# Performance work log

Measured on AMD Instinct MI355X. Metric: run time of the kernel, lower is better.

## Reference

```python
import jax, jax.numpy as jnp
import numpy as np

DEPTH = 3  # chemprop default message passing depth


def setup_inputs() -> dict:
    key = jax.random.key(0)
    ks = jax.random.split(key, 10)
    n_atoms, n_bonds, max_nb, n_mols = 50000, 100000, 6, 2000
    atom_fdim, bond_fdim, hidden = 133, 147, 300
    f_atoms = jax.random.normal(ks[0], (n_atoms, atom_fdim), dtype=jnp.float32)
    f_bonds = jax.random.normal(ks[1], (n_bonds, bond_fdim), dtype=jnp.float32)
    a2b = jax.random.randint(ks[2], (n_atoms, max_nb), 0, n_bonds, dtype=jnp.int32)
    b2a = jax.random.randint(ks[3], (n_bonds,), 0, n_atoms, dtype=jnp.int32)
    b2revb = jax.random.randint(ks[4], (n_bonds,), 0, n_bonds, dtype=jnp.int32)
    mol_id = jnp.sort(jax.random.randint(ks[5], (n_atoms,), 0, n_mols, dtype=jnp.int32))
    W_i = jax.random.normal(ks[6], (bond_fdim, hidden), dtype=jnp.float32) * 0.05
    W_h = jax.random.normal(ks[7], (hidden, hidden), dtype=jnp.float32) * 0.05
    W_o = jax.random.normal(ks[8], (atom_fdim + hidden, hidden), dtype=jnp.float32) * 0.05
    b_o = jnp.zeros((hidden,), dtype=jnp.float32)
    return {"f_atoms": f_atoms, "f_bonds": f_bonds, "a2b": a2b, "b2a": b2a,
            "b2revb": b2revb, "mol_id": mol_id, "n_mols": n_mols,
            "W_i": W_i, "W_h": W_h, "W_o": W_o, "b_o": b_o}


def reference(f_atoms, f_bonds, a2b, b2a, b2revb, mol_id, n_mols, W_i, W_h, W_o, b_o):
    act = jax.nn.relu
    # W_i: bond features -> hidden; message init
    inp = f_bonds @ W_i                      # [n_bonds, h]
    message = act(inp)
    for _ in range(DEPTH - 1):
        nei = message[a2b]                    # [n_atoms, max_nb, h] gather
        a_message = nei.sum(axis=1)           # [n_atoms, h]
        rev = message[b2revb]                 # [n_bonds, h]
        message = a_message[b2a] - rev        # [n_bonds, h]
        message = act(inp + message @ W_h)
    # final atom readout
    a_message = message[a2b].sum(axis=1)      # [n_atoms, h]
    a_input = jnp.concatenate([f_atoms, a_message], axis=1)  # [n_atoms, fa+h]
    atom_hiddens = act(a_input @ W_o + b_o)   # [n_atoms, h]
    # ragged per-molecule mean (a_scope loop -> segment mean)
    sums = jax.ops.segment_sum(atom_hiddens, mol_id, num_segments=n_mols)
    counts = jax.ops.segment_sum(jnp.ones((atom_hiddens.shape[0],), dtype=atom_hiddens.dtype), mol_id, num_segments=n_mols)
    mol_vecs = jnp.where(counts[:, None] > 0, sums / jnp.maximum(counts, 1.0)[:, None], 0.0)
    return mol_vecs
```

## Files before the change

### kernel.cpp

```cpp
#include <hip/hip_runtime.h>
#include <cstddef>

#define H 300
#define RS 304
#define MAXNB 6
#define ASTR 312

typedef __attribute__((ext_vector_type(8)))  short bf16x8;
typedef __attribute__((ext_vector_type(16))) float f32x16;

__device__ __forceinline__ float bf2f(unsigned short u) {
    return __uint_as_float(((unsigned int)u) << 16);
}
__device__ __forceinline__ unsigned short f2bf(float f) {
    unsigned int u = __float_as_uint(f);
    u += 0x7FFFu + ((u >> 16) & 1u);
    return (unsigned short)(u >> 16);
}
__device__ __forceinline__ unsigned int sub2bf(unsigned int a, unsigned int b) {
    float d0 = bf2f((unsigned short)(a & 0xFFFFu)) - bf2f((unsigned short)(b & 0xFFFFu));
    float d1 = bf2f((unsigned short)(a >> 16))     - bf2f((unsigned short)(b >> 16));
    return (unsigned int)f2bf(d0) | ((unsigned int)f2bf(d1) << 16);
}
__device__ __forceinline__ unsigned int relu2(unsigned int w) {
    unsigned int r = w;
    if (w & 0x80000000u) r &= 0x0000FFFFu;
    if (w & 0x00008000u) r &= 0xFFFF0000u;
    return r;
}
__device__ __forceinline__ uint4 relu4(uint4 v) {
    v.x = relu2(v.x); v.y = relu2(v.y); v.z = relu2(v.z); v.w = relu2(v.w);
    return v;
}
__device__ __forceinline__ uint4 subpack4(uint4 a, uint4 b) {
    uint4 r;
    r.x = sub2bf(a.x, b.x); r.y = sub2bf(a.y, b.y);
    r.z = sub2bf(a.z, b.z); r.w = sub2bf(a.w, b.w);
    return r;
}


template<int S>
__global__ void __launch_bounds__(256)
pack_a_f32_c(const float* __restrict__ src, unsigned short* __restrict__ dst,
             int M, int K)
{
    __shared__ unsigned short sm[64 * 152];
    const int m0 = blockIdx.x * 64;
    const int r = threadIdx.x >> 2;
    const int q = threadIdx.x & 3;
    int mv = m0 + r; if (mv >= M) mv = M - 1;
    const float* rowF = src + (size_t)mv * K;
#pragma unroll
    for (int i = 0; i < (S * 4 + 3) / 4; ++i) {
        int c = q + i * 4;
        if (c * 4 < S * 16) {
            unsigned short h[4];
#pragma unroll
            for (int e = 0; e < 4; ++e) {
                int k = c * 4 + e;
                h[e] = (k < K) ? f2bf(rowF[k]) : (unsigned short)0;
            }
            uint2 o;
            o.x = (unsigned int)h[0] | ((unsigned int)h[1] << 16);
            o.y = (unsigned int)h[2] | ((unsigned int)h[3] << 16);
            *(uint2*)&sm[r * 152 + c * 4] = o;
        }
    }
    __syncthreads();
    for (int j = threadIdx.x; j < 2 * S * 64; j += 256) {
        int lane = j & 63;
        int t = j >> 6;
        int s = t % S;
        int mb2 = t / S;
        uint4 v = *(const uint4*)&sm[(mb2 * 32 + (lane & 31)) * 152 + s * 16 + (lane >> 5) * 8];
        int m_blk = blockIdx.x * 2 + mb2;
        *(uint4*)&dst[((size_t)(m_blk * S + s) * 64 + lane) * 8] = v;
    }
}

__device__ __forceinline__ void
pack_b_body(int g, const float* __restrict__ src1, const float* __restrict__ src2,
            unsigned short* __restrict__ dst, int K1, int S1, int K2, int SB)
{
    if (g >= 10 * SB * 64) return;
    int lane = g & 63;
    int t = g >> 6;
    int s = t % SB;
    int n_blk = t / SB;
    int n = n_blk * 32 + (lane & 31);
    unsigned int w[4];
#pragma unroll
    for (int p = 0; p < 4; ++p) {
        unsigned short h[2];
#pragma unroll
        for (int e = 0; e < 2; ++e) {
            int kf = s * 16 + (lane >> 5) * 8 + p * 2 + e;
            float v = 0.0f;
            if (n < H) {
                if (s < S1) {
                    if (kf < K1) v = src1[(size_t)kf * H + n];
                } else {
                    int k2 = kf - S1 * 16;
                    if (k2 < K2) v = src2[(size_t)k2 * H + n];
                }
            }
            h[e] = f2bf(v);
        }
        w[p] = (unsigned int)h[0] | ((unsigned int)h[1] << 16);
    }
    *(uint4*)&dst[(size_t)g * 8] = make_uint4(w[0], w[1], w[2], w[3]);
}

__global__ void __launch_bounds__(256)
pack_b_all(const float* __restrict__ Wi, const float* __restrict__ Wh,
           const float* __restrict__ Wo,
           unsigned short* __restrict__ wih, unsigned short* __restrict__ wh19,
           unsigned short* __restrict__ wo, int bond_fdim, int atom_fdim)
{
    const int B0 = (10 * 30 * 64 + 255) / 256;
    const int B1 = (10 * 19 * 64 + 255) / 256;
    int b = blockIdx.x;
    if (b < B0) {
        pack_b_body(b * 256 + threadIdx.x, Wi, Wh, wih, bond_fdim, 10, H, 30);
    } else if (b < B0 + B1) {
        pack_b_body((b - B0) * 256 + threadIdx.x, Wh, Wh, wh19, H, 19, 0, 19);
    } else {
        pack_b_body((b - B0 - B1) * 256 + threadIdx.x, Wo,
                    Wo + (size_t)atom_fdim * H, wo, atom_fdim, 9, H, 29);
    }
}

template<int RELU>
__global__ void __launch_bounds__(256)
aggregate_row(const unsigned short* __restrict__ msg, const int* __restrict__ a2b,
              unsigned short* __restrict__ amsg, int n_atoms)
{
    int gid = blockIdx.x * 256 + threadIdx.x;
    int total = n_atoms * 38;
    if (gid >= total) return;
    int atom = gid / 38;
    int g8 = gid - atom * 38;
    const int* nb = a2b + atom * MAXNB;
    float sum[8] = {};
#pragma unroll
    for (int j = 0; j < MAXNB; ++j) {
        int b = nb[j];
        uint4 v = *(const uint4*)&msg[(size_t)b * RS + g8 * 8];
        if (RELU) v = relu4(v);
        unsigned int ww[4] = {v.x, v.y, v.z, v.w};
#pragma unroll
        for (int p = 0; p < 4; ++p) {
            sum[p * 2]     += bf2f((unsigned short)(ww[p] & 0xFFFFu));
            sum[p * 2 + 1] += bf2f((unsigned short)(ww[p] >> 16));
        }
    }
    unsigned int ow[4];
#pragma unroll
    for (int p = 0; p < 4; ++p)
        ow[p] = (unsigned int)f2bf(sum[p * 2]) | ((unsigned int)f2bf(sum[p * 2 + 1]) << 16);
    *(uint4*)&amsg[(size_t)atom * RS + g8 * 8] = make_uint4(ow[0], ow[1], ow[2], ow[3]);
}

template<int S1, int S2, int SBL, int MODE, int RELUMSG>
__global__ void __launch_bounds__(640, 8)
gemm_fused(const unsigned short* __restrict__ A1,
           const unsigned short* __restrict__ amsg,
           const unsigned short* __restrict__ msg,
           const int* __restrict__ b2a, const int* __restrict__ b2revb,
           const unsigned short* __restrict__ Bp,
           const float* __restrict__ bias,
           const unsigned short* __restrict__ inp_add,
           const float* __restrict__ Adense, int Kd,
           unsigned short* __restrict__ out, int M)
{
    __shared__ __align__(16) unsigned short smem[64 * ASTR];

    const int lane  = threadIdx.x & 63;
    const int w     = threadIdx.x >> 6;
    const int mrow  = lane & 31;
    const int quad  = lane >> 5;
    const int m0    = blockIdx.x * 64;

    if (threadIdx.x < 512) {
        const int r = threadIdx.x >> 3;
        const int q = threadIdx.x & 7;
        int mm = m0 + r;
        int mv = (mm < M) ? mm : 0;
        if (MODE == 0) {
            if (mm >= M) mv = M - 1;
            const float* rowF = Adense + (size_t)mv * Kd;
#pragma unroll
            for (int i = 0; i < 5; ++i) {
                int c = q + i * 8;
                if (c * 4 < S2 * 16) {
                    unsigned short h[4];
#pragma unroll
                    for (int e = 0; e < 4; ++e) {
                        int k = c * 4 + e;
                        h[e] = (k < Kd) ? f2bf(rowF[k]) : (unsigned short)0;
                    }
                    uint2 o;
                    o.x = (unsigned int)h[0] | ((unsigned int)h[1] << 16);
                    o.y = (unsigned int)h[2] | ((unsigned int)h[3] << 16);
                    *(uint2*)&smem[r * ASTR + c * 4] = o;
                }
            }
        } else if (MODE == 3) {
            const int* nb = b2a + mv * MAXNB;
#pragma unroll
            for (int i = 0; i < 5; ++i) {
                int c = q + i * 8;
                if (c < 38) {
                    float sum[8] = {};
#pragma unroll
                    for (int j = 0; j < MAXNB; ++j) {
                        uint4 v = *(const uint4*)&msg[(size_t)nb[j] * RS + c * 8];
                        unsigned int ww[4] = {v.x, v.y, v.z, v.w};
#pragma unroll
                        for (int p = 0; p < 4; ++p) {
                            sum[p * 2]     += bf2f((unsigned short)(ww[p] & 0xFFFFu));
                            sum[p * 2 + 1] += bf2f((unsigned short)(ww[p] >> 16));
                        }
                    }
                    unsigned int ow[4];
#pragma unroll
                    for (int p = 0; p < 4; ++p)
                        ow[p] = (unsigned int)f2bf(sum[p * 2]) |
                                ((unsigned int)f2bf(sum[p * 2 + 1]) << 16);
                    *(uint4*)&smem[r * ASTR + c * 8] = make_uint4(ow[0], ow[1], ow[2], ow[3]);
                }
            }
        } else {
            const unsigned short* rowA;
            const unsigned short* rowM = nullptr;
            if (MODE == 1) {
                rowA = amsg + (size_t)b2a[mv] * RS;
                rowM = msg  + (size_t)b2revb[mv] * RS;
            } else {
                rowA = amsg + (size_t)mv * RS;
            }
#pragma unroll
            for (int i = 0; i < 5; ++i) {
                int c = q + i * 8;
                if (c < 38) {
                    uint4 o;
                    if (MODE == 1) {
                        uint4 va = *(const uint4*)(rowA + c * 8);
                        uint4 vm = *(const uint4*)(rowM + c * 8);
                        if (RELUMSG) vm = relu4(vm);
                        o = subpack4(va, vm);
                    } else {
                        o = *(const uint4*)(rowA + c * 8);
                    }
                    *(uint4*)&smem[r * ASTR + c * 8] = o;
                }
            }
        }
    }
    __syncthreads();

    f32x16 acc_lo, acc_hi;
#pragma unroll
    for (int i = 0; i < 16; ++i) { acc_lo[i] = 0.0f; acc_hi[i] = 0.0f; }

    const unsigned short* pa1_lo = (S1 > 0)
        ? (A1 + ((size_t)(blockIdx.x * 2 + 0) * S1 * 64 + lane) * 8) : nullptr;
    const unsigned short* pa1_hi = (S1 > 0)
        ? (A1 + ((size_t)(blockIdx.x * 2 + 1) * S1 * 64 + lane) * 8) : nullptr;
    const unsigned short* pb = Bp + ((size_t)w * SBL * 64 + lane) * 8;

    constexpr int STOT = S1 + S2;

    auto loadA = [&](int s, const unsigned short* pa1x, int half) -> bf16x8 {
        if (S1 > 0 && s < S1) return *(const bf16x8*)(pa1x + (size_t)s * 512);
        return *(const bf16x8*)&smem[((half << 5) + mrow) * ASTR + (s - S1) * 16 + quad * 8];
    };

    bf16x8 b0, b1;
    b0 = *(const bf16x8*)(pb);
    if (STOT > 1) b1 = *(const bf16x8*)(pb + 512);

#pragma unroll
    for (int s = 0; s < STOT; s += 2) {
        bf16x8 a_lo = loadA(s, pa1_lo, 0);
        bf16x8 a_hi = loadA(s, pa1_hi, 1);
        acc_lo = __builtin_amdgcn_mfma_f32_32x32x16_bf16(a_lo, b0, acc_lo, 0, 0, 0);
        acc_hi = __builtin_amdgcn_mfma_f32_32x32x16_bf16(a_hi, b0, acc_hi, 0, 0, 0);
        if (s + 2 < STOT) b0 = *(const bf16x8*)(pb + (size_t)(s + 2) * 512);
        if (s + 1 < STOT) {
            bf16x8 a_lo2 = loadA(s + 1, pa1_lo, 0);
            bf16x8 a_hi2 = loadA(s + 1, pa1_hi, 1);
            acc_lo = __builtin_amdgcn_mfma_f32_32x32x16_bf16(a_lo2, b1, acc_lo, 0, 0, 0);
            acc_hi = __builtin_amdgcn_mfma_f32_32x32x16_bf16(a_hi2, b1, acc_hi, 0, 0, 0);
            if (s + 3 < STOT) b1 = *(const bf16x8*)(pb + (size_t)(s + 3) * 512);
        }
    }

    __syncthreads();

    {
        int col = w * 32 + mrow;
        if (col < 308) {
#pragma unroll
            for (int r = 0; r < 16; ++r) {
                int row = (r & 3) + 8 * (r >> 2) + 4 * quad;
                smem[row * 308 + col] = f2bf(acc_lo[r]);
            }
#pragma unroll
            for (int r = 0; r < 16; ++r) {
                int row = 32 + (r & 3) + 8 * (r >> 2) + 4 * quad;
                smem[row * 308 + col] = f2bf(acc_hi[r]);
            }
        }
    }
    __syncthreads();

    for (int idx = threadIdx.x; idx < 64 * 76; idx += 640) {
        int row = idx / 76, gcol = idx - row * 76;
        int mm = m0 + row;
        if (mm >= M) continue;
        int c0 = gcol * 4;
        uint2 raw = *(const uint2*)&smem[row * 308 + c0];
        uint2 o;
        if (MODE == 0) {
            o = raw;
        } else {
            unsigned short h[4] = {(unsigned short)(raw.x & 0xFFFFu), (unsigned short)(raw.x >> 16),
                                   (unsigned short)(raw.y & 0xFFFFu), (unsigned short)(raw.y >> 16)};
            float v[4];
#pragma unroll
            for (int e = 0; e < 4; ++e) v[e] = bf2f(h[e]);
            if (MODE == 1) {
                uint2 iv = *(const uint2*)&inp_add[(size_t)mm * RS + c0];
                v[0] += bf2f((unsigned short)(iv.x & 0xFFFFu));
                v[1] += bf2f((unsigned short)(iv.x >> 16));
                v[2] += bf2f((unsigned short)(iv.y & 0xFFFFu));
                v[3] += bf2f((unsigned short)(iv.y >> 16));
            } else {
#pragma unroll
                for (int e = 0; e < 4; ++e) v[e] += (c0 + e < H) ? bias[c0 + e] : 0.0f;
            }
#pragma unroll
            for (int e = 0; e < 4; ++e) h[e] = f2bf(fmaxf(v[e], 0.0f));
            o.x = (unsigned int)h[0] | ((unsigned int)h[1] << 16);
            o.y = (unsigned int)h[2] | ((unsigned int)h[3] << 16);
        }
        *(uint2*)&out[(size_t)mm * RS + c0] = o;
    }
}

__global__ void __launch_bounds__(128)
segmean_kernel(const unsigned short* __restrict__ ah,
               const int* __restrict__ mol_id, int n_atoms,
               float* __restrict__ out)
{
    int m = blockIdx.x;
    int lo = 0, hi = n_atoms;
    while (lo < hi) { int mid = (lo + hi) >> 1; if (mol_id[mid] < m) lo = mid + 1; else hi = mid; }
    int start = lo;
    hi = n_atoms;
    while (lo < hi) { int mid = (lo + hi) >> 1; if (mol_id[mid] < m + 1) lo = mid + 1; else hi = mid; }
    int end = lo;

    int c = threadIdx.x;
    float a0 = 0.f, a1 = 0.f, a2 = 0.f;
    for (int a = start; a < end; ++a) {
        const unsigned short* row = ah + (size_t)a * RS;
        a0 += bf2f(row[c]);
        a1 += bf2f(row[c + 128]);
        if (c < H - 256) a2 += bf2f(row[c + 256]);
    }
    float inv = (end > start) ? 1.0f / (float)(end - start) : 0.0f;
    float* orow = out + (size_t)m * H;
    orow[c] = a0 * inv;
    orow[c + 128] = a1 * inv;
    if (c < H - 256) orow[c + 256] = a2 * inv;
}

extern "C" void kernel_launch(void* const* d_in, const int* in_sizes, int n_in,
                              void* d_out, int out_size, void* d_ws, size_t ws_size,
                              hipStream_t stream)
{
    const float* f_atoms = (const float*)d_in[0];
    const float* f_bonds = (const float*)d_in[1];
    const int*   a2b     = (const int*)d_in[2];
    const int*   b2a     = (const int*)d_in[3];
    const int*   b2revb  = (const int*)d_in[4];
    const int*   mol_id  = (const int*)d_in[5];
    const float* W_i     = (const float*)d_in[7];
    const float* W_h     = (const float*)d_in[8];
    const float* W_o     = (const float*)d_in[9];
    const float* b_o     = (const float*)d_in[10];

    const int n_atoms   = in_sizes[5];
    const int n_bonds   = in_sizes[3];
    const int atom_fdim = in_sizes[0] / n_atoms;
    const int bond_fdim = in_sizes[1] / n_bonds;
    const int n_mols    = out_size / H;

    const int gAtoms  = (n_atoms + 63) / 64;
    const int gBonds  = (n_bonds + 63) / 64;

    const size_t bondsRS = (size_t)n_bonds * RS;
    const size_t atomsRS = (size_t)n_atoms * RS;
    const size_t wihSz   = 10 * 30 * 512;
    const size_t woSz    = 10 * 29 * 512;
    const size_t wh19Sz  = 10 * 19 * 512;

    unsigned short* inp  = (unsigned short*)d_ws;
    unsigned short* msgB = inp  + bondsRS;
    unsigned short* amsg = msgB + bondsRS;
    unsigned short* wih  = amsg + atomsRS;
    unsigned short* wo   = wih  + wihSz;
    unsigned short* wh19 = wo   + woSz;
    unsigned short* ah   = wh19 + wh19Sz;
    unsigned short* fap  = msgB;

    dim3 blk(256);
    dim3 gblk(640);
    const int aggBlocks = (n_atoms * 38 + 255) / 256;
    const int packBlocks = (10 * 30 * 64 + 255) / 256 + (10 * 19 * 64 + 255) / 256
                         + (10 * 29 * 64 + 255) / 256;

    pack_b_all<<<packBlocks, blk, 0, stream>>>(W_i, W_h, W_o, wih, wh19, wo,
                                               bond_fdim, atom_fdim);

    gemm_fused<0, 10, 30, 0, 0><<<gBonds, gblk, 0, stream>>>(
        nullptr, nullptr, nullptr, nullptr, nullptr, wih, nullptr, nullptr,
        f_bonds, bond_fdim, inp, n_bonds);

    aggregate_row<1><<<aggBlocks, blk, 0, stream>>>(inp, a2b, amsg, n_atoms);
    gemm_fused<0, 19, 19, 1, 1><<<gBonds, gblk, 0, stream>>>(
        nullptr, amsg, inp, b2a, b2revb, wh19, nullptr, inp, nullptr, 0, msgB, n_bonds);

    aggregate_row<0><<<aggBlocks, blk, 0, stream>>>(msgB, a2b, amsg, n_atoms);
    gemm_fused<0, 19, 19, 1, 0><<<gBonds, gblk, 0, stream>>>(
        nullptr, amsg, msgB, b2a, b2revb, wh19, nullptr, inp, nullptr, 0, inp, n_bonds);

    pack_a_f32_c<9><<<gAtoms, blk, 0, stream>>>(f_atoms, fap, n_atoms, atom_fdim);

    gemm_fused<9, 19, 29, 3, 0><<<gAtoms, gblk, 0, stream>>>(
        fap, nullptr, inp, a2b, nullptr, wo, b_o, nullptr,
        nullptr, 0, ah, n_atoms);

    segmean_kernel<<<n_mols, dim3(128), 0, stream>>>(ah, mol_id, n_atoms, (float*)d_out);
}
```

Measured before the change: 473.6 us.

## Fuse segment-sum readout into output GEMM epilogue with atomic accumulation

```diff
diff --git a/kernel.cpp b/kernel.cpp
--- a/kernel.cpp
+++ b/kernel.cpp
@@ -116,18 +116,23 @@
 pack_b_all(const float* __restrict__ Wi, const float* __restrict__ Wh,
            const float* __restrict__ Wo,
            unsigned short* __restrict__ wih, unsigned short* __restrict__ wh19,
-           unsigned short* __restrict__ wo, int bond_fdim, int atom_fdim)
+           unsigned short* __restrict__ wo, int bond_fdim, int atom_fdim,
+           float* __restrict__ osum, int osum4)
 {
     const int B0 = (10 * 30 * 64 + 255) / 256;
     const int B1 = (10 * 19 * 64 + 255) / 256;
+    const int B2 = (10 * 29 * 64 + 255) / 256;
     int b = blockIdx.x;
     if (b < B0) {
         pack_b_body(b * 256 + threadIdx.x, Wi, Wh, wih, bond_fdim, 10, H, 30);
     } else if (b < B0 + B1) {
         pack_b_body((b - B0) * 256 + threadIdx.x, Wh, Wh, wh19, H, 19, 0, 19);
-    } else {
+    } else if (b < B0 + B1 + B2) {
         pack_b_body((b - B0 - B1) * 256 + threadIdx.x, Wo,
                     Wo + (size_t)atom_fdim * H, wo, atom_fdim, 9, H, 29);
+    } else {
+        int idx = (b - B0 - B1 - B2) * 256 + threadIdx.x;
+        if (idx < osum4) ((float4*)osum)[idx] = make_float4(0.f, 0.f, 0.f, 0.f);
     }
 }
 
@@ -172,7 +177,8 @@
            const float* __restrict__ bias,
            const unsigned short* __restrict__ inp_add,
            const float* __restrict__ Adense, int Kd,
-           unsigned short* __restrict__ out, int M)
+           unsigned short* __restrict__ out, int M,
+           const int* __restrict__ mol_idp, float* __restrict__ osum)
 {
     __shared__ __align__(16) unsigned short smem[64 * ASTR];
 
@@ -316,6 +322,50 @@
     }
     __syncthreads();
 
+    if (MODE == 3) {
+        const int g = threadIdx.x / 76;
+        const int c = threadIdx.x - g * 76;
+        if (threadIdx.x < 608 && c < 75) {
+            const int c0 = c * 4;
+            float bb[4];
+#pragma unroll
+            for (int e = 0; e < 4; ++e) bb[e] = bias[c0 + e];
+            float s[4] = {0.f, 0.f, 0.f, 0.f};
+            int curm = -1;
+            for (int rr = g * 8; rr < g * 8 + 8; ++rr) {
+                int mm = m0 + rr;
+                if (mm >= M) break;
+                int mol = mol_idp[mm];
+                if (mol != curm) {
+                    if (curm >= 0) {
+#pragma unroll
+                        for (int e = 0; e < 4; ++e)
+                            if (s[e] != 0.0f)
+                                atomicAdd(&osum[(size_t)curm * H + c0 + e], s[e]);
+                    }
+                    curm = mol;
+#pragma unroll
+                    for (int e = 0; e < 4; ++e) s[e] = 0.0f;
+                }
+                uint2 raw = *(const uint2*)&smem[rr * 308 + c0];
+                unsigned short h[4] = {(unsigned short)(raw.x & 0xFFFFu),
+                                       (unsigned short)(raw.x >> 16),
+                                       (unsigned short)(raw.y & 0xFFFFu),
+                                       (unsigned short)(raw.y >> 16)};
+#pragma unroll
+                for (int e = 0; e < 4; ++e)
+                    s[e] += bf2f(f2bf(fmaxf(bf2f(h[e]) + bb[e], 0.0f)));
+            }
+            if (curm >= 0) {
+#pragma unroll
+                for (int e = 0; e < 4; ++e)
+                    if (s[e] != 0.0f)
+                        atomicAdd(&osum[(size_t)curm * H + c0 + e], s[e]);
+            }
+        }
+        return;
+    }
+
     for (int idx = threadIdx.x; idx < 64 * 76; idx += 640) {
         int row = idx / 76, gcol = idx - row * 76;
         int mm = m0 + row;
@@ -350,10 +400,9 @@
     }
 }
 
-__global__ void __launch_bounds__(128)
-segmean_kernel(const unsigned short* __restrict__ ah,
-               const int* __restrict__ mol_id, int n_atoms,
-               float* __restrict__ out)
+__global__ void __launch_bounds__(64)
+finalize_mean(const int* __restrict__ mol_id, int n_atoms,
+              float* __restrict__ osum)
 {
     int m = blockIdx.x;
     int lo = 0, hi = n_atoms;
@@ -362,20 +411,9 @@
     hi = n_atoms;
     while (lo < hi) { int mid = (lo + hi) >> 1; if (mol_id[mid] < m + 1) lo = mid + 1; else hi = mid; }
     int end = lo;
-
-    int c = threadIdx.x;
-    float a0 = 0.f, a1 = 0.f, a2 = 0.f;
-    for (int a = start; a < end; ++a) {
-        const unsigned short* row = ah + (size_t)a * RS;
-        a0 += bf2f(row[c]);
-        a1 += bf2f(row[c + 128]);
-        if (c < H - 256) a2 += bf2f(row[c + 256]);
-    }
     float inv = (end > start) ? 1.0f / (float)(end - start) : 0.0f;
-    float* orow = out + (size_t)m * H;
-    orow[c] = a0 * inv;
-    orow[c + 128] = a1 * inv;
-    if (c < H - 256) orow[c + 256] = a2 * inv;
+    float* row = osum + (size_t)m * H;
+    for (int k = threadIdx.x; k < H; k += 64) row[k] *= inv;
 }
 
 extern "C" void kernel_launch(void* const* d_in, const int* in_sizes, int n_in,
@@ -414,35 +452,39 @@
     unsigned short* wih  = amsg + atomsRS;
     unsigned short* wo   = wih  + wihSz;
     unsigned short* wh19 = wo   + woSz;
-    unsigned short* ah   = wh19 + wh19Sz;
     unsigned short* fap  = msgB;
 
     dim3 blk(256);
     dim3 gblk(640);
     const int aggBlocks = (n_atoms * 38 + 255) / 256;
+    const int osum4     = out_size / 4;
     const int packBlocks = (10 * 30 * 64 + 255) / 256 + (10 * 19 * 64 + 255) / 256
-                         + (10 * 29 * 64 + 255) / 256;
+                         + (10 * 29 * 64 + 255) / 256
+                         + (osum4 + 255) / 256;
 
     pack_b_all<<<packBlocks, blk, 0, stream>>>(W_i, W_h, W_o, wih, wh19, wo,
-                                               bond_fdim, atom_fdim);
+                                               bond_fdim, atom_fdim,
+                                               (float*)d_out, osum4);
 
     gemm_fused<0, 10, 30, 0, 0><<<gBonds, gblk, 0, stream>>>(
         nullptr, nullptr, nullptr, nullptr, nullptr, wih, nullptr, nullptr,
-        f_bonds, bond_fdim, inp, n_bonds);
+        f_bonds, bond_fdim, inp, n_bonds, nullptr, nullptr);
 
     aggregate_row<1><<<aggBlocks, blk, 0, stream>>>(inp, a2b, amsg, n_atoms);
     gemm_fused<0, 19, 19, 1, 1><<<gBonds, gblk, 0, stream>>>(
-        nullptr, amsg, inp, b2a, b2revb, wh19, nullptr, inp, nullptr, 0, msgB, n_bonds);
+        nullptr, amsg, inp, b2a, b2revb, wh19, nullptr, inp, nullptr, 0,
+        msgB, n_bonds, nullptr, nullptr);
 
     aggregate_row<0><<<aggBlocks, blk, 0, stream>>>(msgB, a2b, amsg, n_atoms);
     gemm_fused<0, 19, 19, 1, 0><<<gBonds, gblk, 0, stream>>>(
-        nullptr, amsg, msgB, b2a, b2revb, wh19, nullptr, inp, nullptr, 0, inp, n_bonds);
+        nullptr, amsg, msgB, b2a, b2revb, wh19, nullptr, inp, nullptr, 0,
+        inp, n_bonds, nullptr, nullptr);
 
     pack_a_f32_c<9><<<gAtoms, blk, 0, stream>>>(f_atoms, fap, n_atoms, atom_fdim);
 
     gemm_fused<9, 19, 29, 3, 0><<<gAtoms, gblk, 0, stream>>>(
         fap, nullptr, inp, a2b, nullptr, wo, b_o, nullptr,
-        nullptr, 0, ah, n_atoms);
-
-    segmean_kernel<<<n_mols, dim3(128), 0, stream>>>(ah, mol_id, n_atoms, (float*)d_out);
-}
+        nullptr, 0, nullptr, n_atoms, mol_id, (float*)d_out);
+
+    finalize_mean<<<n_mols, dim3(64), 0, stream>>>(mol_id, n_atoms, (float*)d_out);
+}
```

Result: no change. 476.7 us (+0.7%).
